# Optimization experiments

Measured on AMD Instinct MI355X. Metric: run time of the kernel, lower is better.

## Reference

```python
import jax, jax.numpy as jnp
import numpy as np

N_NODES = 100000
N_EDGES = 1200000
HIDDEN = 64
N_GRAPHS = 64


def setup_inputs() -> dict:
    key = jax.random.key(0)
    ks = jax.random.split(key, 16)
    H = HIDDEN
    s = 1.0 / np.sqrt(H)
    inp = {
        "x": jax.random.normal(ks[0], (N_NODES,), dtype=jnp.float32),
        "edge_index": jax.random.randint(ks[1], (2, N_EDGES), 0, N_NODES, dtype=jnp.int64),
        "edge_attr": jax.random.normal(ks[2], (N_EDGES, 1), dtype=jnp.float32),
        "batch": jnp.sort(jax.random.randint(ks[3], (N_NODES,), 0, N_GRAPHS, dtype=jnp.int64)),
        # node/edge encoders: Linear(1, H)
        "ne_w": jax.random.normal(ks[4], (1, H), dtype=jnp.float32),
        "ne_b": jnp.zeros((H,), dtype=jnp.float32),
        "ee_w": jax.random.normal(ks[5], (1, H), dtype=jnp.float32),
        "ee_b": jnp.zeros((H,), dtype=jnp.float32),
        # conv1 MLP: Linear(H,H) -> ReLU -> Linear(H,H)
        "c1_w1": jax.random.normal(ks[6], (H, H), dtype=jnp.float32) * s,
        "c1_b1": jnp.zeros((H,), dtype=jnp.float32),
        "c1_w2": jax.random.normal(ks[7], (H, H), dtype=jnp.float32) * s,
        "c1_b2": jnp.zeros((H,), dtype=jnp.float32),
        # conv2 MLP
        "c2_w1": jax.random.normal(ks[8], (H, H), dtype=jnp.float32) * s,
        "c2_b1": jnp.zeros((H,), dtype=jnp.float32),
        "c2_w2": jax.random.normal(ks[9], (H, H), dtype=jnp.float32) * s,
        "c2_b2": jnp.zeros((H,), dtype=jnp.float32),
    }
    return inp


def reference(x, edge_index, edge_attr, batch,
              ne_w, ne_b, ee_w, ee_b,
              c1_w1, c1_b1, c1_w2, c1_b2,
              c2_w1, c2_b1, c2_w2, c2_b2):
    N = x.shape[0]
    src, dst = edge_index[0], edge_index[1]

    h = x.reshape(-1, 1) @ ne_w + ne_b          # [N, H]
    e = edge_attr @ ee_w + ee_b                 # [E, H]

    def gine(h, w1, b1, w2, b2):
        # message: relu(x_src + edge_attr), scatter-add to dst; eps = 0
        m = jax.nn.relu(h[src] + e)             # [E, H]
        agg = jax.ops.segment_sum(m, dst, num_segments=N)
        z = h + agg                             # (1 + eps) * x + agg, eps=0
        return jax.nn.relu(z @ w1 + b1) @ w2 + b2

    h = jax.nn.relu(gine(h, c1_w1, c1_b1, c1_w2, c1_b2))
    h = jax.nn.relu(gine(h, c2_w1, c2_b1, c2_w2, c2_b2))

    # global_mean_pool
    sums = jax.ops.segment_sum(h, batch, num_segments=N_GRAPHS)      # [G, H]
    counts = jax.ops.segment_sum(jnp.ones((N,), h.dtype), batch, num_segments=N_GRAPHS)
    return sums / jnp.clip(counts, 1.0)[:, None]
```

## Files before the change

kernel.cpp:

```cpp
#include <hip/hip_runtime.h>
#include <hip/hip_fp16.h>

constexpr int H = 64;
constexpr int PAD = 68;
constexpr int BSH = 6;
constexpr int EPB = 4096;
constexpr int EPT = EPB / 256;

__device__ inline unsigned pack2(float a, float b) {
    __half2 hh = __floats2half2_rn(a, b);
    return *(unsigned*)&hh;
}
__device__ inline float2 up2(unsigned u) {
    __half2 hh = *(__half2*)&u;
    return __half22float2(hh);
}

__global__ __launch_bounds__(256) void encode_kernel(
    const float* __restrict__ x, const float* __restrict__ nw,
    const float* __restrict__ nb, __half* __restrict__ hout, int N,
    unsigned* __restrict__ zp, int zn)
{
    int idx = blockIdx.x * 256 + threadIdx.x;
    if (idx < zn) zp[idx] = 0u;
    if (idx >= N * 16) return;
    int n = idx >> 4, c = idx & 15;
    float xv = x[n];
    float4 w = ((const float4*)nw)[c];
    float4 b = ((const float4*)nb)[c];
    uint2 r;
    r.x = pack2(fmaf(xv, w.x, b.x), fmaf(xv, w.y, b.y));
    r.y = pack2(fmaf(xv, w.z, b.z), fmaf(xv, w.w, b.w));
    ((uint2*)hout)[idx] = r;
}

__global__ __launch_bounds__(256) void bhist_kernel(
    const int* __restrict__ ei, int* __restrict__ ghist, int E, int NB)
{
    extern __shared__ int lh[];
    for (int b = threadIdx.x; b < NB; b += 256) lh[b] = 0;
    __syncthreads();
    int k0 = blockIdx.x * EPB;
#pragma unroll
    for (int i = 0; i < EPT; ++i) {
        int k = k0 + threadIdx.x + i * 256;
        if (k < E) atomicAdd(&lh[ei[E + k] >> BSH], 1);
    }
    __syncthreads();
    for (int b = threadIdx.x; b < NB; b += 256)
        if (lh[b]) atomicAdd(&ghist[b], lh[b]);
}

__global__ __launch_bounds__(256) void bscan_kernel(
    const int* __restrict__ ghist, int* __restrict__ off,
    int* __restrict__ gcur, int NB)
{
    __shared__ int part[256];
    int t = threadIdx.x;
    const int C = (NB + 255) / 256;
    int loc[16];
    int s = 0;
    for (int j = 0; j < C; ++j) {
        int idx = t * C + j;
        int v = (idx < NB) ? ghist[idx] : 0;
        loc[j] = s; s += v;
    }
    part[t] = s;
    __syncthreads();
    for (int d = 1; d < 256; d <<= 1) {
        int x = (t >= d) ? part[t - d] : 0;
        __syncthreads();
        part[t] += x;
        __syncthreads();
    }
    int base = part[t] - s;
    for (int j = 0; j < C; ++j) {
        int idx = t * C + j;
        if (idx < NB) { int v = base + loc[j]; off[idx] = v; gcur[idx] = v; }
    }
    if (t == 255) off[NB] = part[255];
}

__global__ __launch_bounds__(256) void binscatter_kernel(
    const int* __restrict__ ei, const float* __restrict__ eattr,
    int* __restrict__ gcur, int2* __restrict__ bed, int E, int NB)
{
    extern __shared__ int smem[];
    int2* stage = (int2*)smem;
    int*  A     = smem + 2 * EPB;
    int*  B     = A + NB + 1;
    int*  part  = B + NB;
    int t = threadIdx.x;
    int k0 = blockIdx.x * EPB;

    for (int b = t; b < NB + 1; b += 256) A[b] = 0;
    __syncthreads();

    int dsts[EPT];
#pragma unroll
    for (int i = 0; i < EPT; ++i) {
        int k = k0 + t + i * 256;
        dsts[i] = (k < E) ? ei[E + k] : -1;
        if (dsts[i] >= 0) atomicAdd(&A[dsts[i] >> BSH], 1);
    }
    __syncthreads();

    const int C = (NB + 255) / 256;
    int loc[16];
    int s = 0;
    for (int j = 0; j < C; ++j) {
        int idx = t * C + j;
        int v = (idx < NB) ? A[idx] : 0;
        loc[j] = s; s += v;
    }
    part[t] = s;
    __syncthreads();
    for (int d = 1; d < 256; d <<= 1) {
        int x = (t >= d) ? part[t - d] : 0;
        __syncthreads();
        part[t] += x;
        __syncthreads();
    }
    int base = part[t] - s;
    int tot = part[255];
    for (int j = 0; j < C; ++j) {
        int idx = t * C + j;
        if (idx < NB) { int e = base + loc[j]; A[idx] = e; B[idx] = e; }
    }
    if (t == 255) A[NB] = tot;
    __syncthreads();

#pragma unroll
    for (int i = 0; i < EPT; ++i) {
        if (dsts[i] >= 0) {
            int k = k0 + t + i * 256;
            int b = dsts[i] >> BSH;
            int dl = dsts[i] & 63;
            int slot = atomicAdd(&B[b], 1);
            stage[slot] = make_int2((dl << 17) | ei[k], __float_as_int(eattr[k]));
        }
    }
    __syncthreads();

    for (int b = t; b < NB; b += 256) {
        int c0 = A[b], c1 = B[b];
        if (c1 > c0) B[b] = atomicAdd(&gcur[b], c1 - c0) - c0;
    }
    __syncthreads();

    int s0 = t * EPT;
    int lo = 0, hi = NB;
    while (hi - lo > 1) { int mid = (lo + hi) >> 1; if (A[mid] <= s0) lo = mid; else hi = mid; }
    int b = lo;
#pragma unroll
    for (int i = 0; i < EPT; ++i) {
        int sl = s0 + i;
        if (sl >= tot) break;
        while (sl >= A[b + 1]) ++b;
        bed[B[b] + sl] = stage[sl];
    }
}

__global__ __launch_bounds__(256) void dlsort_kernel(
    int2* __restrict__ bed, const int* __restrict__ off,
    int* __restrict__ nstart, int* __restrict__ nend, int N, int NB)
{
    __shared__ int2 stage[4096];
    __shared__ int hist[64], excl[65], cur[64];
    int t = threadIdx.x, b = blockIdx.x;
    int e0 = off[b], e1 = off[b + 1], cnt = e1 - e0;
    if (t < 64) hist[t] = 0;
    __syncthreads();

    if (cnt <= 4096) {
        for (int i = t; i < cnt; i += 256) {
            int2 r = bed[e0 + i];
            stage[i] = r;
            atomicAdd(&hist[(unsigned)r.x >> 17], 1);
        }
        __syncthreads();
        if (t == 0) {
            int s = 0;
#pragma unroll
            for (int i = 0; i < 64; ++i) { excl[i] = s; s += hist[i]; }
            excl[64] = s;
        }
        __syncthreads();
        if (t < 64) {
            cur[t] = excl[t];
            int n = b * 64 + t;
            if (n < N) { nstart[n] = e0 + excl[t]; nend[n] = e0 + excl[t + 1]; }
        }
        __syncthreads();
        for (int i = t; i < cnt; i += 256) {
            int2 r = stage[i];
            int p = atomicAdd(&cur[(unsigned)r.x >> 17], 1);
            bed[e0 + p] = r;
        }
    } else {
        int n = b * 64 + t;
        if (t < 64 && n < N) { nstart[n] = e0; nend[n] = ~e1; }
    }
}

__global__ __launch_bounds__(256) void gather_kernel(
    const __half* __restrict__ h, const int2* __restrict__ bed,
    const int* __restrict__ nstart, const int* __restrict__ nend,
    const float* __restrict__ ew, const float* __restrict__ eb,
    __half* __restrict__ z, int N)
{
    int lane = threadIdx.x & 63;
    int wid  = threadIdx.x >> 6;
    int n = blockIdx.x * 4 + wid;
    if (n >= N) return;
    float wj = ew[lane], bj = eb[lane];
    int e  = nstart[n];
    int e1 = nend[n];
    float acc = __half2float(h[(size_t)n * H + lane]);

    if (e1 >= 0) {
        while (e1 - e > 16) {
            const int2* p = bed + __builtin_amdgcn_readfirstlane(e);
            int2 r0 = p[0], r1 = p[1], r2 = p[2], r3 = p[3];
            int2 r4 = p[4], r5 = p[5], r6 = p[6], r7 = p[7];
            float v0 = __half2float(h[(size_t)(r0.x & 0x1FFFF) * H + lane]);
            float v1 = __half2float(h[(size_t)(r1.x & 0x1FFFF) * H + lane]);
            float v2 = __half2float(h[(size_t)(r2.x & 0x1FFFF) * H + lane]);
            float v3 = __half2float(h[(size_t)(r3.x & 0x1FFFF) * H + lane]);
            float v4 = __half2float(h[(size_t)(r4.x & 0x1FFFF) * H + lane]);
            float v5 = __half2float(h[(size_t)(r5.x & 0x1FFFF) * H + lane]);
            float v6 = __half2float(h[(size_t)(r6.x & 0x1FFFF) * H + lane]);
            float v7 = __half2float(h[(size_t)(r7.x & 0x1FFFF) * H + lane]);
            acc += fmaxf(fmaf(__int_as_float(r0.y), wj, bj) + v0, 0.f)
                 + fmaxf(fmaf(__int_as_float(r1.y), wj, bj) + v1, 0.f)
                 + fmaxf(fmaf(__int_as_float(r2.y), wj, bj) + v2, 0.f)
                 + fmaxf(fmaf(__int_as_float(r3.y), wj, bj) + v3, 0.f)
                 + fmaxf(fmaf(__int_as_float(r4.y), wj, bj) + v4, 0.f)
                 + fmaxf(fmaf(__int_as_float(r5.y), wj, bj) + v5, 0.f)
                 + fmaxf(fmaf(__int_as_float(r6.y), wj, bj) + v6, 0.f)
                 + fmaxf(fmaf(__int_as_float(r7.y), wj, bj) + v7, 0.f);
            e += 8;
        }
        int r = e1 - e;
        const int2* p = bed + __builtin_amdgcn_readfirstlane(e);
        int2 q0 = p[0],  q1 = p[1],  q2 = p[2],  q3 = p[3];
        int2 q4 = p[4],  q5 = p[5],  q6 = p[6],  q7 = p[7];
        int2 q8 = p[8],  q9 = p[9],  qA = p[10], qB = p[11];
        int2 qC = p[12], qD = p[13], qE = p[14], qF = p[15];
        int s0 = (0  < r) ? (q0.x & 0x1FFFF) : 0;
        int s1 = (1  < r) ? (q1.x & 0x1FFFF) : 0;
        int s2 = (2  < r) ? (q2.x & 0x1FFFF) : 0;
        int s3 = (3  < r) ? (q3.x & 0x1FFFF) : 0;
        int s4 = (4  < r) ? (q4.x & 0x1FFFF) : 0;
        int s5 = (5  < r) ? (q5.x & 0x1FFFF) : 0;
        int s6 = (6  < r) ? (q6.x & 0x1FFFF) : 0;
        int s7 = (7  < r) ? (q7.x & 0x1FFFF) : 0;
        int s8 = (8  < r) ? (q8.x & 0x1FFFF) : 0;
        int s9 = (9  < r) ? (q9.x & 0x1FFFF) : 0;
        int sA = (10 < r) ? (qA.x & 0x1FFFF) : 0;
        int sB = (11 < r) ? (qB.x & 0x1FFFF) : 0;
        int sC = (12 < r) ? (qC.x & 0x1FFFF) : 0;
        int sD = (13 < r) ? (qD.x & 0x1FFFF) : 0;
        int sE = (14 < r) ? (qE.x & 0x1FFFF) : 0;
        int sF = (15 < r) ? (qF.x & 0x1FFFF) : 0;
        float v0 = __half2float(h[(size_t)s0 * H + lane]);
        float v1 = __half2float(h[(size_t)s1 * H + lane]);
        float v2 = __half2float(h[(size_t)s2 * H + lane]);
        float v3 = __half2float(h[(size_t)s3 * H + lane]);
        float v4 = __half2float(h[(size_t)s4 * H + lane]);
        float v5 = __half2float(h[(size_t)s5 * H + lane]);
        float v6 = __half2float(h[(size_t)s6 * H + lane]);
        float v7 = __half2float(h[(size_t)s7 * H + lane]);
        float v8 = __half2float(h[(size_t)s8 * H + lane]);
        float v9 = __half2float(h[(size_t)s9 * H + lane]);
        float vA = __half2float(h[(size_t)sA * H + lane]);
        float vB = __half2float(h[(size_t)sB * H + lane]);
        float vC = __half2float(h[(size_t)sC * H + lane]);
        float vD = __half2float(h[(size_t)sD * H + lane]);
        float vE = __half2float(h[(size_t)sE * H + lane]);
        float vF = __half2float(h[(size_t)sF * H + lane]);
        float m;
        m = fmaxf(fmaf(__int_as_float(q0.y), wj, bj) + v0, 0.f); acc += (0  < r) ? m : 0.f;
        m = fmaxf(fmaf(__int_as_float(q1.y), wj, bj) + v1, 0.f); acc += (1  < r) ? m : 0.f;
        m = fmaxf(fmaf(__int_as_float(q2.y), wj, bj) + v2, 0.f); acc += (2  < r) ? m : 0.f;
        m = fmaxf(fmaf(__int_as_float(q3.y), wj, bj) + v3, 0.f); acc += (3  < r) ? m : 0.f;
        m = fmaxf(fmaf(__int_as_float(q4.y), wj, bj) + v4, 0.f); acc += (4  < r) ? m : 0.f;
        m = fmaxf(fmaf(__int_as_float(q5.y), wj, bj) + v5, 0.f); acc += (5  < r) ? m : 0.f;
        m = fmaxf(fmaf(__int_as_float(q6.y), wj, bj) + v6, 0.f); acc += (6  < r) ? m : 0.f;
        m = fmaxf(fmaf(__int_as_float(q7.y), wj, bj) + v7, 0.f); acc += (7  < r) ? m : 0.f;
        m = fmaxf(fmaf(__int_as_float(q8.y), wj, bj) + v8, 0.f); acc += (8  < r) ? m : 0.f;
        m = fmaxf(fmaf(__int_as_float(q9.y), wj, bj) + v9, 0.f); acc += (9  < r) ? m : 0.f;
        m = fmaxf(fmaf(__int_as_float(qA.y), wj, bj) + vA, 0.f); acc += (10 < r) ? m : 0.f;
        m = fmaxf(fmaf(__int_as_float(qB.y), wj, bj) + vB, 0.f); acc += (11 < r) ? m : 0.f;
        m = fmaxf(fmaf(__int_as_float(qC.y), wj, bj) + vC, 0.f); acc += (12 < r) ? m : 0.f;
        m = fmaxf(fmaf(__int_as_float(qD.y), wj, bj) + vD, 0.f); acc += (13 < r) ? m : 0.f;
        m = fmaxf(fmaf(__int_as_float(qE.y), wj, bj) + vE, 0.f); acc += (14 < r) ? m : 0.f;
        m = fmaxf(fmaf(__int_as_float(qF.y), wj, bj) + vF, 0.f); acc += (15 < r) ? m : 0.f;
    } else {
        int ef = ~e1;
        unsigned mydl = (unsigned)(n & 63);
        for (int ee = e; ee < ef; ++ee) {
            int2 r = bed[ee];
            float v = __half2float(h[(size_t)(r.x & 0x1FFFF) * H + lane]);
            float m = fmaxf(fmaf(__int_as_float(r.y), wj, bj) + v, 0.f);
            acc += (((unsigned)r.x >> 17) == mydl) ? m : 0.f;
        }
    }
    z[(size_t)n * H + lane] = __float2half(acc);
}

__global__ __launch_bounds__(256) void mlp_kernel(
    const __half* __restrict__ z, const float* __restrict__ w1,
    const float* __restrict__ b1, const float* __restrict__ w2,
    const float* __restrict__ b2, __half* __restrict__ out,
    const int* __restrict__ batch, float* __restrict__ sums,
    float* __restrict__ counts, int N, int doPool)
{
    __shared__ float zT[H * PAD];
    __shared__ float wS[H * PAD];
    __shared__ int bseg[64];
    int tid = threadIdx.x;
    int nb = blockIdx.x * 64;

    {
        int i  = tid >> 2;
        int jc = (tid & 3) * 16;
        const float4* s = (const float4*)(w1 + i * H + jc);
        float4* d = (float4*)(wS + i * PAD + jc);
        d[0] = s[0]; d[1] = s[1]; d[2] = s[2]; d[3] = s[3];
    }
    if (doPool && tid < 64) bseg[tid] = (nb + tid < N) ? batch[nb + tid] : -1;
    {
        int nl = tid >> 2;
        int n  = nb + nl;
        int ic = (tid & 3) * 16;
        if (n < N) {
            const uint4* zr = (const uint4*)(z + (size_t)n * H + ic);
            uint4 u0 = zr[0], u1 = zr[1];
            float2 f;
            f = up2(u0.x); zT[(ic+ 0)*PAD+nl]=f.x; zT[(ic+ 1)*PAD+nl]=f.y;
            f = up2(u0.y); zT[(ic+ 2)*PAD+nl]=f.x; zT[(ic+ 3)*PAD+nl]=f.y;
            f = up2(u0.z); zT[(ic+ 4)*PAD+nl]=f.x; zT[(ic+ 5)*PAD+nl]=f.y;
            f = up2(u0.w); zT[(ic+ 6)*PAD+nl]=f.x; zT[(ic+ 7)*PAD+nl]=f.y;
            f = up2(u1.x); zT[(ic+ 8)*PAD+nl]=f.x; zT[(ic+ 9)*PAD+nl]=f.y;
            f = up2(u1.y); zT[(ic+10)*PAD+nl]=f.x; zT[(ic+11)*PAD+nl]=f.y;
            f = up2(u1.z); zT[(ic+12)*PAD+nl]=f.x; zT[(ic+13)*PAD+nl]=f.y;
            f = up2(u1.w); zT[(ic+14)*PAD+nl]=f.x; zT[(ic+15)*PAD+nl]=f.y;
        } else {
#pragma unroll
            for (int m = 0; m < 16; ++m)
                zT[(ic + m) * PAD + nl] = 0.f;
        }
    }
    __syncthreads();

    int tj = tid & 15, tn = tid >> 4;
    int j0 = tj * 4, n0 = tn * 4;

    float acc[4][4] = {};
#pragma unroll 4
    for (int i = 0; i < H; ++i) {
        float4 a = *(const float4*)(zT + i * PAD + n0);
        float4 b = *(const float4*)(wS + i * PAD + j0);
        float av[4] = {a.x, a.y, a.z, a.w};
        float bv[4] = {b.x, b.y, b.z, b.w};
#pragma unroll
        for (int p = 0; p < 4; ++p)
#pragma unroll
            for (int q = 0; q < 4; ++q)
                acc[p][q] = fmaf(av[p], bv[q], acc[p][q]);
    }
    float4 bb1 = *(const float4*)(b1 + j0);
    float u[4][4];
#pragma unroll
    for (int p = 0; p < 4; ++p) {
        u[p][0] = fmaxf(acc[p][0] + bb1.x, 0.f);
        u[p][1] = fmaxf(acc[p][1] + bb1.y, 0.f);
        u[p][2] = fmaxf(acc[p][2] + bb1.z, 0.f);
        u[p][3] = fmaxf(acc[p][3] + bb1.w, 0.f);
    }
    __syncthreads();

#pragma unroll
    for (int p = 0; p < 4; ++p)
#pragma unroll
        for (int q = 0; q < 4; ++q)
            zT[(j0 + q) * PAD + (n0 + p)] = u[p][q];
    {
        int i  = tid >> 2;
        int jc = (tid & 3) * 16;
        const float4* s = (const float4*)(w2 + i * H + jc);
        float4* d = (float4*)(wS + i * PAD + jc);
        d[0] = s[0]; d[1] = s[1]; d[2] = s[2]; d[3] = s[3];
    }
    __syncthreads();

    float acc2[4][4] = {};
#pragma unroll 4
    for (int i = 0; i < H; ++i) {
        float4 a = *(const float4*)(zT + i * PAD + n0);
        float4 b = *(const float4*)(wS + i * PAD + j0);
        float av[4] = {a.x, a.y, a.z, a.w};
        float bv[4] = {b.x, b.y, b.z, b.w};
#pragma unroll
        for (int p = 0; p < 4; ++p)
#pragma unroll
            for (int q = 0; q < 4; ++q)
                acc2[p][q] = fmaf(av[p], bv[q], acc2[p][q]);
    }
    float4 bb2 = *(const float4*)(b2 + j0);

    if (!doPool) {
#pragma unroll
        for (int p = 0; p < 4; ++p) {
            int n = nb + n0 + p;
            if (n < N) {
                uint2 r;
                r.x = pack2(fmaxf(acc2[p][0] + bb2.x, 0.f),
                            fmaxf(acc2[p][1] + bb2.y, 0.f));
                r.y = pack2(fmaxf(acc2[p][2] + bb2.z, 0.f),
                            fmaxf(acc2[p][3] + bb2.w, 0.f));
                *(uint2*)(out + (size_t)n * H + j0) = r;
            }
        }
    } else {
        __syncthreads();
#pragma unroll
        for (int p = 0; p < 4; ++p) {
            zT[(n0 + p) * PAD + j0 + 0] = fmaxf(acc2[p][0] + bb2.x, 0.f);
            zT[(n0 + p) * PAD + j0 + 1] = fmaxf(acc2[p][1] + bb2.y, 0.f);
            zT[(n0 + p) * PAD + j0 + 2] = fmaxf(acc2[p][2] + bb2.z, 0.f);
            zT[(n0 + p) * PAD + j0 + 3] = fmaxf(acc2[p][3] + bb2.w, 0.f);
        }
        __syncthreads();
        if (tid < 64) {
            int j = tid;
            float acc0 = 0.f; int cnt = 0; int cur = bseg[0];
            for (int k = 0; k < 64; ++k) {
                int g = bseg[k];
                if (g < 0) break;
                if (g != cur) {
                    atomicAdd(sums + cur * H + j, acc0);
                    if (j == 0) atomicAdd(counts + cur, (float)cnt);
                    acc0 = 0.f; cnt = 0; cur = g;
                }
                acc0 += zT[k * PAD + j];
                cnt++;
            }
            if (cnt > 0) {
                atomicAdd(sums + cur * H + j, acc0);
                if (j == 0) atomicAdd(counts + cur, (float)cnt);
            }
        }
    }
}

__global__ void div_kernel(const float* __restrict__ sums,
                           const float* __restrict__ counts,
                           float* __restrict__ out)
{
    int g = blockIdx.x, j = threadIdx.x;
    out[g * H + j] = sums[g * H + j] / fmaxf(counts[g], 1.0f);
}

extern "C" void kernel_launch(void* const* d_in, const int* in_sizes, int n_in,
                              void* d_out, int out_size, void* d_ws, size_t ws_size,
                              hipStream_t stream)
{
    const float* x     = (const float*)d_in[0];
    const int*   ei    = (const int*)d_in[1];
    const float* eattr = (const float*)d_in[2];
    const int*   batch = (const int*)d_in[3];
    const float* ne_w  = (const float*)d_in[4];
    const float* ne_b  = (const float*)d_in[5];
    const float* ee_w  = (const float*)d_in[6];
    const float* ee_b  = (const float*)d_in[7];
    const float* c1w1  = (const float*)d_in[8];
    const float* c1b1  = (const float*)d_in[9];
    const float* c1w2  = (const float*)d_in[10];
    const float* c1b2  = (const float*)d_in[11];
    const float* c2w1  = (const float*)d_in[12];
    const float* c2b1  = (const float*)d_in[13];
    const float* c2w2  = (const float*)d_in[14];
    const float* c2b2  = (const float*)d_in[15];

    const int N = in_sizes[0];
    const int E = in_sizes[2];
    const int NB = (N + 63) >> BSH;

    char* w = (char*)d_ws;
    __half* h   = (__half*)w;            w += (size_t)N * H * sizeof(__half);
    __half* z   = (__half*)w;            w += (size_t)N * H * sizeof(__half);
    float* sums = (float*)w;             w += 64 * H * sizeof(float);
    float* counts = (float*)w;           w += 64 * sizeof(float);
    int* ghist  = (int*)w;               w += (size_t)NB * sizeof(int);
    int* off    = (int*)w;               w += (size_t)(NB + 1) * sizeof(int);
    int* gcur   = (int*)w;               w += (size_t)NB * sizeof(int);
    int* nstart = (int*)w;               w += (size_t)N * sizeof(int);
    int* nend   = (int*)w;               w += (size_t)N * sizeof(int);
    uintptr_t p = ((uintptr_t)w + 15) & ~(uintptr_t)15;
    int2* bed   = (int2*)p;

    const int eGrid = (E + EPB - 1) / EPB;
    const int mlpGrid = (N + 63) / 64;

    size_t histLds = (size_t)NB * sizeof(int);
    size_t scatLds = (size_t)(2 * EPB + (NB + 1) + NB + 256) * sizeof(int);

    const int zeroN = 64 * H + 64 + NB;
    encode_kernel<<<(N * 16 + 255) / 256, 256, 0, stream>>>(
        x, ne_w, ne_b, h, N, (unsigned*)sums, zeroN);

    bhist_kernel<<<eGrid, 256, histLds, stream>>>(ei, ghist, E, NB);
    bscan_kernel<<<1, 256, 0, stream>>>(ghist, off, gcur, NB);
    binscatter_kernel<<<eGrid, 256, scatLds, stream>>>(ei, eattr, gcur, bed, E, NB);
    dlsort_kernel<<<NB, 256, 0, stream>>>(bed, off, nstart, nend, N, NB);

    const int gatherGrid = (N + 3) / 4;

    gather_kernel<<<gatherGrid, 256, 0, stream>>>(h, bed, nstart, nend, ee_w, ee_b, z, N);
    mlp_kernel<<<mlpGrid, 256, 0, stream>>>(z, c1w1, c1b1, c1w2, c1b2, h,
                                            batch, sums, counts, N, 0);

    gather_kernel<<<gatherGrid, 256, 0, stream>>>(h, bed, nstart, nend, ee_w, ee_b, z, N);
    mlp_kernel<<<mlpGrid, 256, 0, stream>>>(z, c2w1, c2b1, c2w2, c2b2, (__half*)nullptr,
                                            batch, sums, counts, N, 1);

    div_kernel<<<64, 64, 0, stream>>>(sums, counts, (float*)d_out);
}
```

Before: 211.5 us.

## Run node MLP on MFMA fp16 matrix cores with prepacked weight fragments

Replaces the fp32 FMA-tiled shared-memory GEMMs in the MLP kernel with __builtin_amdgcn_mfma_f32_16x16x32_f16 calls. A new wpack kernel converts the four weight matrices once per call into fp16 MFMA B-fragment layout, so each wave loads them straight from global memory. The z input is read directly as A fragments and the hidden activation is staged through a small fp16 LDS tile. This removes the weight staging, the transpose and the scalar FMA loops, in exchange for fp16 rounding of weights and the intermediate activation. There is also no bounds check on z loads for the last partial block.

```diff
diff --git a/kernel.cpp b/kernel.cpp
--- a/kernel.cpp
+++ b/kernel.cpp
@@ -2,18 +2,17 @@
 #include <hip/hip_fp16.h>
 
 constexpr int H = 64;
-constexpr int PAD = 68;
 constexpr int BSH = 6;
 constexpr int EPB = 4096;
 constexpr int EPT = EPB / 256;
+constexpr int US = 72;
+
+typedef _Float16 half8 __attribute__((ext_vector_type(8)));
+typedef float f32x4 __attribute__((ext_vector_type(4)));
 
 __device__ inline unsigned pack2(float a, float b) {
     __half2 hh = __floats2half2_rn(a, b);
     return *(unsigned*)&hh;
-}
-__device__ inline float2 up2(unsigned u) {
-    __half2 hh = *(__half2*)&u;
-    return __half22float2(hh);
 }
 
 __global__ __launch_bounds__(256) void encode_kernel(
@@ -32,6 +31,25 @@
     r.x = pack2(fmaf(xv, w.x, b.x), fmaf(xv, w.y, b.y));
     r.y = pack2(fmaf(xv, w.z, b.z), fmaf(xv, w.w, b.w));
     ((uint2*)hout)[idx] = r;
+}
+
+__global__ __launch_bounds__(512) void wpack_kernel(
+    const float* __restrict__ w1, const float* __restrict__ w2,
+    const float* __restrict__ w3, const float* __restrict__ w4,
+    half8* __restrict__ f)
+{
+    const float* w = (blockIdx.x == 0) ? w1 : (blockIdx.x == 1) ? w2
+                   : (blockIdx.x == 2) ? w3 : w4;
+    half8* dst = f + blockIdx.x * 512;
+    int t = threadIdx.x;
+    int lane = t & 63, grp = t >> 6;
+    int tj = grp >> 1, ks = grp & 1;
+    int col = tj * 16 + (lane & 15);
+    int k0 = ks * 32 + ((lane >> 4) << 3);
+    half8 v;
+#pragma unroll
+    for (int m = 0; m < 8; ++m) v[m] = (_Float16)w[(k0 + m) * H + col];
+    dst[t] = v;
 }
 
 __global__ __launch_bounds__(256) void bhist_kernel(
@@ -310,127 +328,81 @@
 }
 
 __global__ __launch_bounds__(256) void mlp_kernel(
-    const __half* __restrict__ z, const float* __restrict__ w1,
-    const float* __restrict__ b1, const float* __restrict__ w2,
-    const float* __restrict__ b2, __half* __restrict__ out,
-    const int* __restrict__ batch, float* __restrict__ sums,
-    float* __restrict__ counts, int N, int doPool)
-{
-    __shared__ float zT[H * PAD];
-    __shared__ float wS[H * PAD];
+    const __half* __restrict__ z, const half8* __restrict__ wf,
+    const float* __restrict__ b1, const float* __restrict__ b2,
+    __half* __restrict__ out, const int* __restrict__ batch,
+    float* __restrict__ sums, float* __restrict__ counts, int N, int doPool)
+{
+    __shared__ _Float16 uS[64 * US];
     __shared__ int bseg[64];
-    int tid = threadIdx.x;
+    int tid = threadIdx.x, lane = tid & 63, w = tid >> 6;
     int nb = blockIdx.x * 64;
-
-    {
-        int i  = tid >> 2;
-        int jc = (tid & 3) * 16;
-        const float4* s = (const float4*)(w1 + i * H + jc);
-        float4* d = (float4*)(wS + i * PAD + jc);
-        d[0] = s[0]; d[1] = s[1]; d[2] = s[2]; d[3] = s[3];
-    }
+    int lo = lane & 15, hi = lane >> 4;
     if (doPool && tid < 64) bseg[tid] = (nb + tid < N) ? batch[nb + tid] : -1;
-    {
-        int nl = tid >> 2;
-        int n  = nb + nl;
-        int ic = (tid & 3) * 16;
-        if (n < N) {
-            const uint4* zr = (const uint4*)(z + (size_t)n * H + ic);
-            uint4 u0 = zr[0], u1 = zr[1];
-            float2 f;
-            f = up2(u0.x); zT[(ic+ 0)*PAD+nl]=f.x; zT[(ic+ 1)*PAD+nl]=f.y;
-            f = up2(u0.y); zT[(ic+ 2)*PAD+nl]=f.x; zT[(ic+ 3)*PAD+nl]=f.y;
-            f = up2(u0.z); zT[(ic+ 4)*PAD+nl]=f.x; zT[(ic+ 5)*PAD+nl]=f.y;
-            f = up2(u0.w); zT[(ic+ 6)*PAD+nl]=f.x; zT[(ic+ 7)*PAD+nl]=f.y;
-            f = up2(u1.x); zT[(ic+ 8)*PAD+nl]=f.x; zT[(ic+ 9)*PAD+nl]=f.y;
-            f = up2(u1.y); zT[(ic+10)*PAD+nl]=f.x; zT[(ic+11)*PAD+nl]=f.y;
-            f = up2(u1.z); zT[(ic+12)*PAD+nl]=f.x; zT[(ic+13)*PAD+nl]=f.y;
-            f = up2(u1.w); zT[(ic+14)*PAD+nl]=f.x; zT[(ic+15)*PAD+nl]=f.y;
-        } else {
-#pragma unroll
-            for (int m = 0; m < 16; ++m)
-                zT[(ic + m) * PAD + nl] = 0.f;
-        }
-    }
-    __syncthreads();
-
-    int tj = tid & 15, tn = tid >> 4;
-    int j0 = tj * 4, n0 = tn * 4;
-
-    float acc[4][4] = {};
-#pragma unroll 4
-    for (int i = 0; i < H; ++i) {
-        float4 a = *(const float4*)(zT + i * PAD + n0);
-        float4 b = *(const float4*)(wS + i * PAD + j0);
-        float av[4] = {a.x, a.y, a.z, a.w};
-        float bv[4] = {b.x, b.y, b.z, b.w};
-#pragma unroll
-        for (int p = 0; p < 4; ++p)
-#pragma unroll
-            for (int q = 0; q < 4; ++q)
-                acc[p][q] = fmaf(av[p], bv[q], acc[p][q]);
-    }
-    float4 bb1 = *(const float4*)(b1 + j0);
-    float u[4][4];
-#pragma unroll
-    for (int p = 0; p < 4; ++p) {
-        u[p][0] = fmaxf(acc[p][0] + bb1.x, 0.f);
-        u[p][1] = fmaxf(acc[p][1] + bb1.y, 0.f);
-        u[p][2] = fmaxf(acc[p][2] + bb1.z, 0.f);
-        u[p][3] = fmaxf(acc[p][3] + bb1.w, 0.f);
-    }
-    __syncthreads();
-
-#pragma unroll
-    for (int p = 0; p < 4; ++p)
-#pragma unroll
-        for (int q = 0; q < 4; ++q)
-            zT[(j0 + q) * PAD + (n0 + p)] = u[p][q];
-    {
-        int i  = tid >> 2;
-        int jc = (tid & 3) * 16;
-        const float4* s = (const float4*)(w2 + i * H + jc);
-        float4* d = (float4*)(wS + i * PAD + jc);
-        d[0] = s[0]; d[1] = s[1]; d[2] = s[2]; d[3] = s[3];
-    }
-    __syncthreads();
-
-    float acc2[4][4] = {};
-#pragma unroll 4
-    for (int i = 0; i < H; ++i) {
-        float4 a = *(const float4*)(zT + i * PAD + n0);
-        float4 b = *(const float4*)(wS + i * PAD + j0);
-        float av[4] = {a.x, a.y, a.z, a.w};
-        float bv[4] = {b.x, b.y, b.z, b.w};
-#pragma unroll
-        for (int p = 0; p < 4; ++p)
-#pragma unroll
-            for (int q = 0; q < 4; ++q)
-                acc2[p][q] = fmaf(av[p], bv[q], acc2[p][q]);
-    }
-    float4 bb2 = *(const float4*)(b2 + j0);
+
+    const _Float16* zp = (const _Float16*)z + (size_t)(nb + w * 16 + lo) * H + hi * 8;
+    half8 a0 = *(const half8*)(zp);
+    half8 a1 = *(const half8*)(zp + 32);
+    const half8* w1f = wf + lane;
+    f32x4 c0 = {0.f, 0.f, 0.f, 0.f}, c1 = c0, c2 = c0, c3 = c0;
+    c0 = __builtin_amdgcn_mfma_f32_16x16x32_f16(a0, w1f[0 * 64], c0, 0, 0, 0);
+    c0 = __builtin_amdgcn_mfma_f32_16x16x32_f16(a1, w1f[1 * 64], c0, 0, 0, 0);
+    c1 = __builtin_amdgcn_mfma_f32_16x16x32_f16(a0, w1f[2 * 64], c1, 0, 0, 0);
+    c1 = __builtin_amdgcn_mfma_f32_16x16x32_f16(a1, w1f[3 * 64], c1, 0, 0, 0);
+    c2 = __builtin_amdgcn_mfma_f32_16x16x32_f16(a0, w1f[4 * 64], c2, 0, 0, 0);
+    c2 = __builtin_amdgcn_mfma_f32_16x16x32_f16(a1, w1f[5 * 64], c2, 0, 0, 0);
+    c3 = __builtin_amdgcn_mfma_f32_16x16x32_f16(a0, w1f[6 * 64], c3, 0, 0, 0);
+    c3 = __builtin_amdgcn_mfma_f32_16x16x32_f16(a1, w1f[7 * 64], c3, 0, 0, 0);
+
+    float bv0 = b1[0 * 16 + lo], bv1 = b1[1 * 16 + lo];
+    float bv2 = b1[2 * 16 + lo], bv3 = b1[3 * 16 + lo];
+    int ur = (w * 16 + hi * 4) * US + lo;
+#pragma unroll
+    for (int r = 0; r < 4; ++r) {
+        uS[ur + r * US + 0 * 16] = (_Float16)fmaxf(c0[r] + bv0, 0.f);
+        uS[ur + r * US + 1 * 16] = (_Float16)fmaxf(c1[r] + bv1, 0.f);
+        uS[ur + r * US + 2 * 16] = (_Float16)fmaxf(c2[r] + bv2, 0.f);
+        uS[ur + r * US + 3 * 16] = (_Float16)fmaxf(c3[r] + bv3, 0.f);
+    }
+    __syncthreads();
+
+    const _Float16* up = uS + (w * 16 + lo) * US + hi * 8;
+    half8 u0 = *(const half8*)(up);
+    half8 u1 = *(const half8*)(up + 32);
+    const half8* w2f = wf + 512 + lane;
+    f32x4 d0 = {0.f, 0.f, 0.f, 0.f}, d1 = d0, d2 = d0, d3 = d0;
+    d0 = __builtin_amdgcn_mfma_f32_16x16x32_f16(u0, w2f[0 * 64], d0, 0, 0, 0);
+    d0 = __builtin_amdgcn_mfma_f32_16x16x32_f16(u1, w2f[1 * 64], d0, 0, 0, 0);
+    d1 = __builtin_amdgcn_mfma_f32_16x16x32_f16(u0, w2f[2 * 64], d1, 0, 0, 0);
+    d1 = __builtin_amdgcn_mfma_f32_16x16x32_f16(u1, w2f[3 * 64], d1, 0, 0, 0);
+    d2 = __builtin_amdgcn_mfma_f32_16x16x32_f16(u0, w2f[4 * 64], d2, 0, 0, 0);
+    d2 = __builtin_amdgcn_mfma_f32_16x16x32_f16(u1, w2f[5 * 64], d2, 0, 0, 0);
+    d3 = __builtin_amdgcn_mfma_f32_16x16x32_f16(u0, w2f[6 * 64], d3, 0, 0, 0);
+    d3 = __builtin_amdgcn_mfma_f32_16x16x32_f16(u1, w2f[7 * 64], d3, 0, 0, 0);
+
+    float cb0 = b2[0 * 16 + lo], cb1 = b2[1 * 16 + lo];
+    float cb2 = b2[2 * 16 + lo], cb3 = b2[3 * 16 + lo];
 
     if (!doPool) {
 #pragma unroll
-        for (int p = 0; p < 4; ++p) {
-            int n = nb + n0 + p;
+        for (int r = 0; r < 4; ++r) {
+            int n = nb + w * 16 + hi * 4 + r;
             if (n < N) {
-                uint2 r;
-                r.x = pack2(fmaxf(acc2[p][0] + bb2.x, 0.f),
-                            fmaxf(acc2[p][1] + bb2.y, 0.f));
-                r.y = pack2(fmaxf(acc2[p][2] + bb2.z, 0.f),
-                            fmaxf(acc2[p][3] + bb2.w, 0.f));
-                *(uint2*)(out + (size_t)n * H + j0) = r;
+                __half* o = out + (size_t)n * H + lo;
+                o[0 * 16] = __float2half(fmaxf(d0[r] + cb0, 0.f));
+                o[1 * 16] = __float2half(fmaxf(d1[r] + cb1, 0.f));
+                o[2 * 16] = __float2half(fmaxf(d2[r] + cb2, 0.f));
+                o[3 * 16] = __float2half(fmaxf(d3[r] + cb3, 0.f));
             }
         }
     } else {
         __syncthreads();
 #pragma unroll
-        for (int p = 0; p < 4; ++p) {
-            zT[(n0 + p) * PAD + j0 + 0] = fmaxf(acc2[p][0] + bb2.x, 0.f);
-            zT[(n0 + p) * PAD + j0 + 1] = fmaxf(acc2[p][1] + bb2.y, 0.f);
-            zT[(n0 + p) * PAD + j0 + 2] = fmaxf(acc2[p][2] + bb2.z, 0.f);
-            zT[(n0 + p) * PAD + j0 + 3] = fmaxf(acc2[p][3] + bb2.w, 0.f);
+        for (int r = 0; r < 4; ++r) {
+            uS[ur + r * US + 0 * 16] = (_Float16)fmaxf(d0[r] + cb0, 0.f);
+            uS[ur + r * US + 1 * 16] = (_Float16)fmaxf(d1[r] + cb1, 0.f);
+            uS[ur + r * US + 2 * 16] = (_Float16)fmaxf(d2[r] + cb2, 0.f);
+            uS[ur + r * US + 3 * 16] = (_Float16)fmaxf(d3[r] + cb3, 0.f);
         }
         __syncthreads();
         if (tid < 64) {
@@ -444,7 +416,7 @@
                     if (j == 0) atomicAdd(counts + cur, (float)cnt);
                     acc0 = 0.f; cnt = 0; cur = g;
                 }
-                acc0 += zT[k * PAD + j];
+                acc0 += (float)uS[k * US + j];
                 cnt++;
             }
             if (cnt > 0) {
@@ -499,6 +471,8 @@
     int* nstart = (int*)w;               w += (size_t)N * sizeof(int);
     int* nend   = (int*)w;               w += (size_t)N * sizeof(int);
     uintptr_t p = ((uintptr_t)w + 15) & ~(uintptr_t)15;
+    half8* wfrag = (half8*)p;
+    p += 2048 * sizeof(half8);
     int2* bed   = (int2*)p;
 
     const int eGrid = (E + EPB - 1) / EPB;
@@ -511,6 +485,7 @@
     encode_kernel<<<(N * 16 + 255) / 256, 256, 0, stream>>>(
         x, ne_w, ne_b, h, N, (unsigned*)sums, zeroN);
 
+    wpack_kernel<<<4, 512, 0, stream>>>(c1w1, c1w2, c2w1, c2w2, wfrag);
     bhist_kernel<<<eGrid, 256, histLds, stream>>>(ei, ghist, E, NB);
     bscan_kernel<<<1, 256, 0, stream>>>(ghist, off, gcur, NB);
     binscatter_kernel<<<eGrid, 256, scatLds, stream>>>(ei, eattr, gcur, bed, E, NB);
@@ -519,11 +494,11 @@
     const int gatherGrid = (N + 3) / 4;
 
     gather_kernel<<<gatherGrid, 256, 0, stream>>>(h, bed, nstart, nend, ee_w, ee_b, z, N);
-    mlp_kernel<<<mlpGrid, 256, 0, stream>>>(z, c1w1, c1b1, c1w2, c1b2, h,
+    mlp_kernel<<<mlpGrid, 256, 0, stream>>>(z, wfrag, c1b1, c1b2, h,
                                             batch, sums, counts, N, 0);
 
     gather_kernel<<<gatherGrid, 256, 0, stream>>>(h, bed, nstart, nend, ee_w, ee_b, z, N);
-    mlp_kernel<<<mlpGrid, 256, 0, stream>>>(z, c2w1, c2b1, c2w2, c2b2, (__half*)nullptr,
+    mlp_kernel<<<mlpGrid, 256, 0, stream>>>(z, wfrag + 1024, c2b1, c2b2, (__half*)nullptr,
                                             batch, sums, counts, N, 1);
 
     div_kernel<<<64, 64, 0, stream>>>(sums, counts, (float*)d_out);
```

New measurement: 180.6 us, median of 2. 14.6% less time.
